# Optimization experiments

Measured on AMD Instinct MI355X. Metric: run time of the kernel, lower is better.

The kernel has to match this reference:

```python
import jax, jax.numpy as jnp
import numpy as np
import math

D = 1024
H = 16
B = 4
N = 2048


def setup_inputs() -> dict:
    key = jax.random.key(0)
    ks = jax.random.split(key, 10)
    scale_qkv = 0.01
    def kaiming_uniform(k, shape, scale):
        # attenuated_kaiming_uniform_: fan_in = shape[1], gain for leaky_relu a=sqrt(5)
        fan_in = shape[1]
        gain = math.sqrt(2.0 / (1 + 5.0))
        bound = math.sqrt(3.0) * gain * scale / math.sqrt(fan_in)
        return jax.random.uniform(k, shape, jnp.float32, -bound, bound)
    return {
        "x_q": jax.random.normal(ks[0], (B, N, D), jnp.float32),
        "x_kv": jax.random.normal(ks[1], (B, N, D), jnp.float32),
        "Wq": kaiming_uniform(ks[2], (D, D), scale_qkv),
        "bq": jnp.zeros((D,), jnp.float32),
        "Wk": kaiming_uniform(ks[3], (D, D), scale_qkv),
        "bk": jnp.zeros((D,), jnp.float32),
        "Wv": kaiming_uniform(ks[4], (D, D), scale_qkv),
        "bv": jnp.zeros((D,), jnp.float32),
        "Wo": kaiming_uniform(ks[5], (D, D), 1.0),
        "bo": jnp.zeros((D,), jnp.float32),
    }


def reference(x_q, x_kv, Wq, bq, Wk, bk, Wv, bv, Wo, bo):
    bs, n, d = x_q.shape
    hd = d // H  # head dim
    # torch Linear: y = x @ W^T + b
    q = x_q @ Wq.T + bq
    k = x_kv @ Wk.T + bk
    v = x_kv @ Wv.T + bv
    # reshape to [bs, H, n, hd]
    q = q.reshape(bs, n, H, hd).transpose(0, 2, 1, 3)
    k = k.reshape(bs, n, H, hd).transpose(0, 2, 1, 3)
    v = v.reshape(bs, n, H, hd).transpose(0, 2, 1, 3)
    scores = jnp.einsum("bhqd,bhkd->bhqk", q, k) / math.sqrt(hd)
    seq_ids = jnp.arange(n)
    causal = (seq_ids[None, :] <= seq_ids[:, None]).astype(scores.dtype)  # [n, n]
    scores = scores + (1.0 - causal) * -10000.0
    probs = jax.nn.softmax(scores, axis=-1)
    out = jnp.einsum("bhqk,bhkd->bhqd", probs, v)
    out = out.transpose(0, 2, 1, 3).reshape(bs, n, d)
    return out @ Wo.T + bo
```

## Files before the change

### kernel.cpp

```cpp
#include <hip/hip_runtime.h>

typedef unsigned short u16;
typedef unsigned int u32;
typedef __attribute__((ext_vector_type(8))) short short8;
typedef __attribute__((ext_vector_type(4))) float f32x4;

#define ASYNC_CP16(gsrc, ldst) \
  __builtin_amdgcn_global_load_lds((__attribute__((address_space(1))) void*)(gsrc), \
                                   (__attribute__((address_space(3))) void*)(ldst), 16, 0, 0)

static __device__ __forceinline__ u16 f2bf(float f) {
  u32 u = __builtin_bit_cast(u32, f);
  u = u + 0x7fffu + ((u >> 16) & 1u);
  return (u16)(u >> 16);
}
static __device__ __forceinline__ u32 pk2(float a, float b) {
  return (u32)f2bf(a) | ((u32)f2bf(b) << 16);
}
static __device__ __forceinline__ u32 pk2r(float a, float b) {
  u32 ua = __builtin_bit_cast(u32, a) + 0x8000u;
  u32 ub = __builtin_bit_cast(u32, b) + 0x8000u;
  return __builtin_amdgcn_perm(ub, ua, 0x07060302);
}

__global__ __launch_bounds__(256) void convert_all(
    const float* __restrict__ xq, const float* __restrict__ xkv,
    const float* __restrict__ wq, const float* __restrict__ wk,
    const float* __restrict__ wv, const float* __restrict__ wo,
    u16* __restrict__ dst)
{
  long i = ((long)blockIdx.x * 256 + threadIdx.x) * 4;
  const float* s; long o;
  if      (i < 8388608)  { s = xq;  o = i; }
  else if (i < 16777216) { s = xkv; o = i - 8388608; }
  else if (i < 17825792) { s = wq;  o = i - 16777216; }
  else if (i < 18874368) { s = wk;  o = i - 17825792; }
  else if (i < 19922944) { s = wv;  o = i - 18874368; }
  else                   { s = wo;  o = i - 19922944; }
  float4 v = *(const float4*)(s + o);
  uint2 pkv; pkv.x = pk2(v.x, v.y); pkv.y = pk2(v.z, v.w);
  *(uint2*)(dst + i) = pkv;
}

template<int EPI>
__global__ __launch_bounds__(256)
void gemm_k(const u16* __restrict__ Axq, const u16* __restrict__ Axkv,
            const u16* __restrict__ W0, const u16* __restrict__ W1, const u16* __restrict__ W2,
            const float* __restrict__ b0, const float* __restrict__ b1, const float* __restrict__ b2,
            u16* __restrict__ Qo, u16* __restrict__ Ko, u16* __restrict__ Vo,
            float* __restrict__ Fo)
{
  __shared__ u16 lsa[128*32];
  __shared__ u16 lsb[128*32];
  const int tid = threadIdx.x;
  const int w = tid >> 6, lane = tid & 63;
  const int wr = w >> 1, wc = w & 1;
  const int bm = blockIdx.x, bn = blockIdx.y, z = blockIdx.z;
  const int l15 = lane & 15, l4 = lane >> 4;

  const u16* A; const u16* W; const float* bias;
  if (EPI == 0) {
    A    = (z == 0) ? Axq : Axkv;
    W    = (z == 0) ? W0 : (z == 1) ? W1 : W2;
    bias = (z == 0) ? b0 : (z == 1) ? b1 : b2;
  } else {
    A = Axq; W = W0; bias = b0;
  }
  const u16* Ag = A + (long)bm*128*1024;
  const u16* Wg = W + (long)bn*128*1024;

  f32x4 acc[4][4];
#pragma unroll
  for (int i = 0; i < 4; ++i)
#pragma unroll
    for (int j = 0; j < 4; ++j)
      acc[i][j] = (f32x4){0.f,0.f,0.f,0.f};

  for (int k0 = 0; k0 < 1024; k0 += 32) {
    __syncthreads();
#pragma unroll
    for (int c = 0; c < 2; ++c) {
      int tp = c*256 + tid;
      int row = tp >> 2, col = (tp & 3) * 8;
      ASYNC_CP16(Ag + (long)row*1024 + k0 + col, &lsa[tp*8]);
      ASYNC_CP16(Wg + (long)row*1024 + k0 + col, &lsb[tp*8]);
    }
    __syncthreads();
    short8 af[4], bfr[4];
#pragma unroll
    for (int i = 0; i < 4; ++i)
      af[i] = *(const short8*)&lsa[(wr*64 + i*16 + l15)*32 + l4*8];
#pragma unroll
    for (int j = 0; j < 4; ++j)
      bfr[j] = *(const short8*)&lsb[(wc*64 + j*16 + l15)*32 + l4*8];
#pragma unroll
    for (int i = 0; i < 4; ++i)
#pragma unroll
      for (int j = 0; j < 4; ++j)
        acc[i][j] = __builtin_amdgcn_mfma_f32_16x16x32_bf16(af[i], bfr[j], acc[i][j], 0, 0, 0);
  }

#pragma unroll
  for (int j = 0; j < 4; ++j) {
    const int colg = bn*128 + wc*64 + j*16 + l15;
    const float bb = bias[colg];
#pragma unroll
    for (int i = 0; i < 4; ++i) {
      const int rowg = bm*128 + wr*64 + i*16 + l4*4;
      if (EPI == 1) {
#pragma unroll
        for (int r = 0; r < 4; ++r)
          Fo[(long)(rowg + r)*1024 + colg] = acc[i][j][r] + bb;
      } else {
        const int b  = rowg >> 11, n0 = rowg & 2047;
        const int h  = colg >> 6,  c  = colg & 63;
        const int bh = b*16 + h;
        const long hb = (long)bh*131072 + (long)(n0 >> 7)*8192;
        if (z == 0) {
#pragma unroll
          for (int r = 0; r < 4; ++r)
            Qo[((long)bh*2048 + n0 + r)*64 + c] = f2bf((acc[i][j][r] + bb) * 0.18033688f);
        } else if (z == 1) {
          const long base = hb + (long)(c >> 3)*1024 + (n0 & 127)*8 + (c & 7);
#pragma unroll
          for (int r = 0; r < 4; ++r)
            Ko[base + r*8] = f2bf(acc[i][j][r] + bb);
        } else {
          const long base = hb + (long)((n0 & 127) >> 3)*512 + (long)c*8 + (n0 & 7);
          uint2 pkv;
          pkv.x = pk2(acc[i][j][0] + bb, acc[i][j][1] + bb);
          pkv.y = pk2(acc[i][j][2] + bb, acc[i][j][3] + bb);
          *(uint2*)(Vo + base) = pkv;
        }
      }
    }
  }
}

__global__ __launch_bounds__(512, 4)
void attn_k(const u16* __restrict__ Q, const u16* __restrict__ K,
            const u16* __restrict__ V, u16* __restrict__ AO)
{
  __shared__ u16 lk[2][8192];
  __shared__ u16 lv[2][8192];
  __shared__ u16 lp[8][1024];
  const int tid = threadIdx.x;
  const int w = tid >> 6, lane = tid & 63;
  const int l15 = lane & 15, l4 = lane >> 4;
  const int qt = (gridDim.x - 1) - blockIdx.x;
  const int bh = blockIdx.y;
  const int q0 = qt*128;
  const int qg = q0 + w*16 + l15;
  const u16* Qh = Q + (long)bh*131072;
  const u16* Kh = K + (long)bh*131072;
  const u16* Vh = V + (long)bh*131072;

  short8 qf[2];
#pragma unroll
  for (int ks = 0; ks < 2; ++ks)
    qf[ks] = *(const short8*)&Qh[(long)qg*64 + ks*32 + l4*8];

  f32x4 o[4];
#pragma unroll
  for (int nt = 0; nt < 4; ++nt) o[nt] = (f32x4){0.f,0.f,0.f,0.f};
  float rsum = 0.f;

  u16* pw = &lp[w][0];
  const int swz_q = (l15 & 7);
  const int ktmax = qt;

#pragma unroll
  for (int c = 0; c < 2; ++c) {
    int tp = c*512 + tid;
    ASYNC_CP16(Kh + tp*8, &lk[0][tp*8]);
    ASYNC_CP16(Vh + tp*8, &lv[0][tp*8]);
  }

  for (int kt = 0; kt <= ktmax; ++kt) {
    const int cur = kt & 1;
    if (kt < ktmax) {
      const long off = (long)(kt + 1)*8192;
#pragma unroll
      for (int c = 0; c < 2; ++c) {
        int tp = c*512 + tid;
        ASYNC_CP16(Kh + off + tp*8, &lk[cur^1][tp*8]);
        ASYNC_CP16(Vh + off + tp*8, &lv[cur^1][tp*8]);
      }
      asm volatile("s_waitcnt vmcnt(4)" ::: "memory");
    } else {
      asm volatile("s_waitcnt vmcnt(0)" ::: "memory");
    }
    __builtin_amdgcn_s_barrier();

    const u16* lkc = &lk[cur][0];
    const u16* lvc = &lv[cur][0];

    f32x4 s[8];
#pragma unroll
    for (int nt = 0; nt < 8; ++nt) s[nt] = (f32x4){0.f,0.f,0.f,0.f};
#pragma unroll
    for (int ks = 0; ks < 2; ++ks)
#pragma unroll
      for (int nt = 0; nt < 8; ++nt) {
        short8 kf = *(const short8*)&lkc[(ks*4 + l4)*1024 + (nt*16 + l15)*8];
        s[nt] = __builtin_amdgcn_mfma_f32_16x16x32_bf16(kf, qf[ks], s[nt], 0, 0, 0);
      }

    if (kt == ktmax) {
      const int kb = kt*128 + l4*4;
#pragma unroll
      for (int nt = 0; nt < 8; ++nt)
#pragma unroll
        for (int r = 0; r < 4; ++r)
          if (kb + nt*16 + r > qg) s[nt][r] = -1e30f;
    }

    u32 pk[8][2];
#pragma unroll
    for (int nt = 0; nt < 8; ++nt) {
      float p0 = __builtin_amdgcn_exp2f(s[nt][0]);
      float p1 = __builtin_amdgcn_exp2f(s[nt][1]);
      float p2 = __builtin_amdgcn_exp2f(s[nt][2]);
      float p3 = __builtin_amdgcn_exp2f(s[nt][3]);
      rsum += (p0 + p1) + (p2 + p3);
      pk[nt][0] = pk2r(p0, p1);
      pk[nt][1] = pk2r(p2, p3);
    }

#pragma unroll
    for (int h = 0; h < 2; ++h) {
#pragma unroll
      for (int ntl = 0; ntl < 4; ++ntl) {
        const int chunk = ntl*2 + (l4 >> 1);
        const int swz = chunk ^ swz_q;
        uint2 pr; pr.x = pk[4*h + ntl][0]; pr.y = pk[4*h + ntl][1];
        *(uint2*)&pw[l15*64 + swz*8 + (l4 & 1)*4] = pr;
      }
#pragma unroll
      for (int ksl = 0; ksl < 2; ++ksl) {
        const int swz = (ksl*4 + l4) ^ swz_q;
        short8 pf = *(const short8*)&pw[l15*64 + swz*8];
        const int ksg = h*2 + ksl;
#pragma unroll
        for (int nt = 0; nt < 4; ++nt) {
          short8 vf = *(const short8*)&lvc[(ksg*4 + l4)*512 + (nt*16 + l15)*8];
          o[nt] = __builtin_amdgcn_mfma_f32_16x16x32_bf16(vf, pf, o[nt], 0, 0, 0);
        }
      }
    }

    asm volatile("" ::: "memory");
    __builtin_amdgcn_s_barrier();
  }

  rsum += __shfl_xor(rsum, 16, 64);
  rsum += __shfl_xor(rsum, 32, 64);

  const int b = bh >> 4, h = bh & 15;
  const float inv = 1.0f / rsum;
  const long tok = (long)b*2048 + qg;
#pragma unroll
  for (int nt = 0; nt < 4; ++nt) {
    uint2 pkv;
    pkv.x = pk2(o[nt][0]*inv, o[nt][1]*inv);
    pkv.y = pk2(o[nt][2]*inv, o[nt][3]*inv);
    *(uint2*)&AO[tok*1024 + h*64 + nt*16 + l4*4] = pkv;
  }
}

extern "C" void kernel_launch(void* const* d_in, const int* in_sizes, int n_in,
                              void* d_out, int out_size, void* d_ws, size_t ws_size,
                              hipStream_t stream)
{
  const float* xq  = (const float*)d_in[0];
  const float* xkv = (const float*)d_in[1];
  const float* Wq  = (const float*)d_in[2];
  const float* bq  = (const float*)d_in[3];
  const float* Wk  = (const float*)d_in[4];
  const float* bk  = (const float*)d_in[5];
  const float* Wv  = (const float*)d_in[6];
  const float* bv  = (const float*)d_in[7];
  const float* Wo  = (const float*)d_in[8];
  const float* bo  = (const float*)d_in[9];

  u16* ws    = (u16*)d_ws;
  u16* xq_b  = ws;
  u16* xkv_b = xq_b  + (1l<<23);
  u16* wq_b  = xkv_b + (1l<<23);
  u16* wk_b  = wq_b  + (1l<<20);
  u16* wv_b  = wk_b  + (1l<<20);
  u16* wo_b  = wv_b  + (1l<<20);
  u16* Qb    = wo_b  + (1l<<20);
  u16* Kb    = Qb    + (1l<<23);
  u16* Vb    = Kb    + (1l<<23);
  u16* Ab    = Vb    + (1l<<23);

  convert_all<<<20480, 256, 0, stream>>>(xq, xkv, Wq, Wk, Wv, Wo, ws);
  gemm_k<0><<<dim3(64,8,3), 256, 0, stream>>>(xq_b, xkv_b, wq_b, wk_b, wv_b,
                                              bq, bk, bv, Qb, Kb, Vb, nullptr);
  attn_k<<<dim3(16,64), 512, 0, stream>>>(Qb, Kb, Vb, Ab);
  gemm_k<1><<<dim3(64,8,1), 256, 0, stream>>>(Ab, nullptr, wo_b, nullptr, nullptr,
                                              bo, nullptr, nullptr,
                                              nullptr, nullptr, nullptr,
                                              (float*)d_out);
}
```

Before: 323.5 us.

## Rework attention inner loop with 32x32 MFMA and register P via permlane swap

Switches the attention kernel from 16x16x32 to 32x32x16 bf16 MFMA tiles. Each wave now handles 32 queries and half of the 128-key tile, and the two key halves are reduced through LDS at the end. The P matrix is repacked in registers with v_cvt_pk_bf16_f32 and v_permlane32_swap, which removes the per-wave LDS round trip for probabilities. Waves whose key half lies entirely above the causal diagonal skip the final tile. In exchange it adds an end-of-kernel cross-wave reduction with extra syncs and uses more accumulator registers.

```diff
diff --git a/kernel.cpp b/kernel.cpp
--- a/kernel.cpp
+++ b/kernel.cpp
@@ -4,6 +4,8 @@
 typedef unsigned int u32;
 typedef __attribute__((ext_vector_type(8))) short short8;
 typedef __attribute__((ext_vector_type(4))) float f32x4;
+typedef __attribute__((ext_vector_type(16))) float f32x16;
+typedef __attribute__((ext_vector_type(4))) unsigned u32x4;
 
 #define ASYNC_CP16(gsrc, ldst) \
   __builtin_amdgcn_global_load_lds((__attribute__((address_space(1))) void*)(gsrc), \
@@ -17,10 +19,13 @@
 static __device__ __forceinline__ u32 pk2(float a, float b) {
   return (u32)f2bf(a) | ((u32)f2bf(b) << 16);
 }
-static __device__ __forceinline__ u32 pk2r(float a, float b) {
-  u32 ua = __builtin_bit_cast(u32, a) + 0x8000u;
-  u32 ub = __builtin_bit_cast(u32, b) + 0x8000u;
-  return __builtin_amdgcn_perm(ub, ua, 0x07060302);
+static __device__ __forceinline__ u32 cvtpk(float lo, float hi) {
+  u32 r;
+  asm("v_cvt_pk_bf16_f32 %0, %1, %2" : "=v"(r) : "v"(lo), "v"(hi));
+  return r;
+}
+static __device__ __forceinline__ void plswap(u32 &a, u32 &b) {
+  asm("v_permlane32_swap_b32 %0, %1" : "+v"(a), "+v"(b));
 }
 
 __global__ __launch_bounds__(256) void convert_all(
@@ -143,30 +148,29 @@
 {
   __shared__ u16 lk[2][8192];
   __shared__ u16 lv[2][8192];
-  __shared__ u16 lp[8][1024];
   const int tid = threadIdx.x;
   const int w = tid >> 6, lane = tid & 63;
-  const int l15 = lane & 15, l4 = lane >> 4;
+  const int l31 = lane & 31, l5 = lane >> 5;
+  const int wq = w & 3, hh = w >> 2;
   const int qt = (gridDim.x - 1) - blockIdx.x;
   const int bh = blockIdx.y;
   const int q0 = qt*128;
-  const int qg = q0 + w*16 + l15;
+  const int qg = q0 + wq*32 + l31;
   const u16* Qh = Q + (long)bh*131072;
   const u16* Kh = K + (long)bh*131072;
   const u16* Vh = V + (long)bh*131072;
 
-  short8 qf[2];
-#pragma unroll
-  for (int ks = 0; ks < 2; ++ks)
-    qf[ks] = *(const short8*)&Qh[(long)qg*64 + ks*32 + l4*8];
-
-  f32x4 o[4];
-#pragma unroll
-  for (int nt = 0; nt < 4; ++nt) o[nt] = (f32x4){0.f,0.f,0.f,0.f};
+  short8 qf[4];
+#pragma unroll
+  for (int ks = 0; ks < 4; ++ks)
+    qf[ks] = *(const short8*)&Qh[(long)qg*64 + ks*16 + l5*8];
+
+  f32x16 o0 = (f32x16)0.0f;
+  f32x16 o1 = (f32x16)0.0f;
   float rsum = 0.f;
 
-  u16* pw = &lp[w][0];
-  const int swz_q = (l15 & 7);
+  const int koff = l5*2048 + l31*16;
+  const int voff = l5*1024 + l31*16;
   const int ktmax = qt;
 
 #pragma unroll
@@ -192,60 +196,54 @@
     }
     __builtin_amdgcn_s_barrier();
 
-    const u16* lkc = &lk[cur][0];
-    const u16* lvc = &lv[cur][0];
-
-    f32x4 s[8];
-#pragma unroll
-    for (int nt = 0; nt < 8; ++nt) s[nt] = (f32x4){0.f,0.f,0.f,0.f};
-#pragma unroll
-    for (int ks = 0; ks < 2; ++ks)
-#pragma unroll
-      for (int nt = 0; nt < 8; ++nt) {
-        short8 kf = *(const short8*)&lkc[(ks*4 + l4)*1024 + (nt*16 + l15)*8];
-        s[nt] = __builtin_amdgcn_mfma_f32_16x16x32_bf16(kf, qf[ks], s[nt], 0, 0, 0);
+    const char* lkc = (const char*)lk + cur*16384;
+    const char* lvc = (const char*)lv + cur*16384;
+
+    const bool active = !(kt == ktmax && hh*64 > wq*32 + 31);
+    if (active) {
+      short8 pf[4];
+#pragma unroll
+      for (int sbl = 0; sbl < 2; ++sbl) {
+        f32x16 sa = (f32x16)0.0f;
+#pragma unroll
+        for (int ks = 0; ks < 4; ++ks) {
+          short8 kf = *(const short8*)(lkc + koff + ks*4096 + (hh*2 + sbl)*512);
+          sa = __builtin_amdgcn_mfma_f32_32x32x16_bf16(kf, qf[ks], sa, 0, 0, 0);
+        }
+        if (kt == ktmax) {
+          const int kb = kt*128 + hh*64 + sbl*32 + 4*l5;
+#pragma unroll
+          for (int g = 0; g < 4; ++g)
+#pragma unroll
+            for (int rr = 0; rr < 4; ++rr)
+              if (kb + 8*g + rr > qg) sa[4*g + rr] = -1e30f;
+        }
+        float p[16];
+#pragma unroll
+        for (int r = 0; r < 16; ++r) p[r] = __builtin_amdgcn_exp2f(sa[r]);
+#pragma unroll
+        for (int g = 0; g < 4; ++g)
+          rsum += (p[4*g] + p[4*g+1]) + (p[4*g+2] + p[4*g+3]);
+        u32 cc[4][2];
+#pragma unroll
+        for (int g = 0; g < 4; ++g) {
+          cc[g][0] = cvtpk(p[4*g],   p[4*g+1]);
+          cc[g][1] = cvtpk(p[4*g+2], p[4*g+3]);
+        }
+        plswap(cc[0][0], cc[1][0]); plswap(cc[0][1], cc[1][1]);
+        plswap(cc[2][0], cc[3][0]); plswap(cc[2][1], cc[3][1]);
+        u32x4 pw0 = {cc[0][0], cc[0][1], cc[1][0], cc[1][1]};
+        u32x4 pw1 = {cc[2][0], cc[2][1], cc[3][0], cc[3][1]};
+        pf[sbl*2]     = __builtin_bit_cast(short8, pw0);
+        pf[sbl*2 + 1] = __builtin_bit_cast(short8, pw1);
       }
-
-    if (kt == ktmax) {
-      const int kb = kt*128 + l4*4;
-#pragma unroll
-      for (int nt = 0; nt < 8; ++nt)
-#pragma unroll
-        for (int r = 0; r < 4; ++r)
-          if (kb + nt*16 + r > qg) s[nt][r] = -1e30f;
-    }
-
-    u32 pk[8][2];
-#pragma unroll
-    for (int nt = 0; nt < 8; ++nt) {
-      float p0 = __builtin_amdgcn_exp2f(s[nt][0]);
-      float p1 = __builtin_amdgcn_exp2f(s[nt][1]);
-      float p2 = __builtin_amdgcn_exp2f(s[nt][2]);
-      float p3 = __builtin_amdgcn_exp2f(s[nt][3]);
-      rsum += (p0 + p1) + (p2 + p3);
-      pk[nt][0] = pk2r(p0, p1);
-      pk[nt][1] = pk2r(p2, p3);
-    }
-
-#pragma unroll
-    for (int h = 0; h < 2; ++h) {
-#pragma unroll
-      for (int ntl = 0; ntl < 4; ++ntl) {
-        const int chunk = ntl*2 + (l4 >> 1);
-        const int swz = chunk ^ swz_q;
-        uint2 pr; pr.x = pk[4*h + ntl][0]; pr.y = pk[4*h + ntl][1];
-        *(uint2*)&pw[l15*64 + swz*8 + (l4 & 1)*4] = pr;
-      }
-#pragma unroll
-      for (int ksl = 0; ksl < 2; ++ksl) {
-        const int swz = (ksl*4 + l4) ^ swz_q;
-        short8 pf = *(const short8*)&pw[l15*64 + swz*8];
-        const int ksg = h*2 + ksl;
-#pragma unroll
-        for (int nt = 0; nt < 4; ++nt) {
-          short8 vf = *(const short8*)&lvc[(ksg*4 + l4)*512 + (nt*16 + l15)*8];
-          o[nt] = __builtin_amdgcn_mfma_f32_16x16x32_bf16(vf, pf, o[nt], 0, 0, 0);
-        }
+#pragma unroll
+      for (int j = 0; j < 4; ++j) {
+        const char* vb = lvc + voff + (hh*4 + j)*2048;
+        short8 vf0 = *(const short8*)(vb);
+        o0 = __builtin_amdgcn_mfma_f32_32x32x16_bf16(vf0, pf[j], o0, 0, 0, 0);
+        short8 vf1 = *(const short8*)(vb + 512);
+        o1 = __builtin_amdgcn_mfma_f32_32x32x16_bf16(vf1, pf[j], o1, 0, 0, 0);
       }
     }
 
@@ -253,18 +251,57 @@
     __builtin_amdgcn_s_barrier();
   }
 
-  rsum += __shfl_xor(rsum, 16, 64);
-  rsum += __shfl_xor(rsum, 32, 64);
-
-  const int b = bh >> 4, h = bh & 15;
-  const float inv = 1.0f / rsum;
-  const long tok = (long)b*2048 + qg;
-#pragma unroll
-  for (int nt = 0; nt < 4; ++nt) {
-    uint2 pkv;
-    pkv.x = pk2(o[nt][0]*inv, o[nt][1]*inv);
-    pkv.y = pk2(o[nt][2]*inv, o[nt][3]*inv);
-    *(uint2*)&AO[tok*1024 + h*64 + nt*16 + l4*4] = pkv;
+  __syncthreads();
+  float* exf = (float*)&lk[0][0];
+  float* rxf = (float*)&lv[0][0];
+  const int sw = lane & 7;
+  float* xb = exf + wq*2048 + lane*32;
+
+  if (hh == 1) {
+#pragma unroll
+    for (int c = 0; c < 4; ++c) {
+      f32x4 v; v[0]=o0[c*4]; v[1]=o0[c*4+1]; v[2]=o0[c*4+2]; v[3]=o0[c*4+3];
+      *(f32x4*)(xb + ((c ^ sw)*4)) = v;
+    }
+#pragma unroll
+    for (int c = 0; c < 4; ++c) {
+      f32x4 v; v[0]=o1[c*4]; v[1]=o1[c*4+1]; v[2]=o1[c*4+2]; v[3]=o1[c*4+3];
+      *(f32x4*)(xb + (((c+4) ^ sw)*4)) = v;
+    }
+    rxf[wq*64 + lane] = rsum;
+  }
+  __syncthreads();
+  if (hh == 0) {
+    float rt = rsum + rxf[wq*64 + lane];
+    rt += __shfl_xor(rt, 32, 64);
+    const float inv = 1.0f / rt;
+#pragma unroll
+    for (int c = 0; c < 4; ++c) {
+      f32x4 v = *(const f32x4*)(xb + ((c ^ sw)*4));
+      o0[c*4] += v[0]; o0[c*4+1] += v[1]; o0[c*4+2] += v[2]; o0[c*4+3] += v[3];
+    }
+#pragma unroll
+    for (int c = 0; c < 4; ++c) {
+      f32x4 v = *(const f32x4*)(xb + (((c+4) ^ sw)*4));
+      o1[c*4] += v[0]; o1[c*4+1] += v[1]; o1[c*4+2] += v[2]; o1[c*4+3] += v[3];
+    }
+    const int b = bh >> 4, h = bh & 15;
+    const long tok = (long)b*2048 + qg;
+    u16* dst = AO + tok*1024 + h*64;
+#pragma unroll
+    for (int g = 0; g < 4; ++g) {
+      uint2 pkv;
+      pkv.x = pk2(o0[4*g]*inv,   o0[4*g+1]*inv);
+      pkv.y = pk2(o0[4*g+2]*inv, o0[4*g+3]*inv);
+      *(uint2*)(dst + 8*g + 4*l5) = pkv;
+    }
+#pragma unroll
+    for (int g = 0; g < 4; ++g) {
+      uint2 pkv;
+      pkv.x = pk2(o1[4*g]*inv,   o1[4*g+1]*inv);
+      pkv.y = pk2(o1[4*g+2]*inv, o1[4*g+3]*inv);
+      *(uint2*)(dst + 32 + 8*g + 4*l5) = pkv;
+    }
   }
 }
 
```

After: 305.7 us. -5.5%, faster.
